# Kernel tuning notes

Measured on AMD Instinct MI355X. Metric: run time of the kernel, lower is better.

Reference implementation:

```python
import jax, jax.numpy as jnp
import numpy as np

N_ATOM = 100000
N_BOND = 400000
N_GLOBAL = 5000
IN = 128
OUT = 128
HEADS = 2
NEG_SLOPE = 0.2
BN_EPS = 1e-5


def setup_inputs() -> dict:
    key = jax.random.key(0)
    ks = jax.random.split(key, 12)
    atom_feats = jax.random.normal(ks[0], (N_ATOM, IN), jnp.float32)
    bond_feats = jax.random.normal(ks[1], (N_BOND, IN), jnp.float32)
    global_feats = jax.random.normal(ks[2], (N_GLOBAL, IN), jnp.float32)
    W_atom = jax.random.normal(ks[3], (IN, OUT * HEADS), jnp.float32) * 0.05
    W_bond = jax.random.normal(ks[4], (IN, OUT * HEADS), jnp.float32) * 0.05
    W_global = jax.random.normal(ks[5], (IN, OUT * HEADS), jnp.float32) * 0.05
    attn_l = jax.random.normal(ks[6], (1, HEADS, OUT), jnp.float32) * 0.1
    attn_r = jax.random.normal(ks[7], (1, HEADS, OUT), jnp.float32) * 0.1
    bn_gamma = jnp.ones((OUT,), jnp.float32)
    bn_beta = jnp.zeros((OUT,), jnp.float32)
    bond_src = jax.random.randint(ks[8], (N_BOND,), 0, N_ATOM, jnp.int32)
    # ensure every atom appears as a bond destination at least once (DGL-like semantics)
    bond_dst = jnp.concatenate([
        jnp.arange(N_ATOM, dtype=jnp.int32),
        jax.random.randint(ks[9], (N_BOND - N_ATOM,), 0, N_ATOM, jnp.int32),
    ])
    g2a_src = jax.random.randint(ks[10], (N_ATOM,), 0, N_GLOBAL, jnp.int32)
    return dict(atom_feats=atom_feats, bond_feats=bond_feats, global_feats=global_feats,
                W_atom=W_atom, W_bond=W_bond, W_global=W_global,
                attn_l=attn_l, attn_r=attn_r, bn_gamma=bn_gamma, bn_beta=bn_beta,
                bond_src=bond_src, bond_dst=bond_dst, g2a_src=g2a_src)


def _fwd(atom_feats, bond_feats, global_feats, W_atom, W_bond, W_global,
         attn_l, attn_r, bn_gamma, bn_beta, bond_src, bond_dst, g2a_src):
    lrelu = lambda x: jax.nn.leaky_relu(x, NEG_SLOPE)
    # projections -> [*, H, D]
    h = (atom_feats @ W_atom).reshape(-1, HEADS, OUT)      # [N,H,D]
    e = (bond_feats @ W_bond).reshape(-1, HEADS, OUT)      # [E,H,D]
    u = (global_feats @ W_global).reshape(-1, HEADS, OUT)  # [G,H,D]
    er = (h * attn_r).sum(-1)    # [N,H]
    el_h = (h * attn_l).sum(-1)  # [N,H]
    el_e = (e * attn_l).sum(-1)  # [E,H]
    el_u = (u * attn_l).sum(-1)  # [G,H]
    er_dst = er[bond_dst]                      # [E,H]
    eh = lrelu(el_h[bond_src] + er_dst)        # bond: u_add_v
    ee = lrelu(el_e + er_dst)                  # bond: e_add_v
    eu = lrelu(el_u[g2a_src] + er)             # g2a: u_add_v (dst = arange(N))
    # numerically-stable edge softmax over both edge types per destination atom
    emax_b = jax.ops.segment_max(jnp.maximum(eh, ee), bond_dst, num_segments=N_ATOM)
    emax = jnp.maximum(emax_b, eu)             # [N,H]
    eh = jnp.exp(eh - emax[bond_dst])
    ee = jnp.exp(ee - emax[bond_dst])
    eu = jnp.exp(eu - emax)
    esum = jax.ops.segment_sum(eh + ee, bond_dst, num_segments=N_ATOM) + eu  # [N,H]
    esum_dst = esum[bond_dst]
    alpha_h = eh / esum_dst    # [E,H]
    alpha_e = ee / esum_dst
    alpha_u = eu / esum        # [N,H]
    msg = h[bond_src] * alpha_h[:, :, None] + e * alpha_e[:, :, None]  # [E,H,D]
    out = jax.ops.segment_sum(msg, bond_dst, num_segments=N_ATOM)
    out = out + u[g2a_src] * alpha_u[:, :, None]   # [N,H,D]
    hN = out.mean(axis=1)                           # mean over heads -> [N,D]
    # BatchNorm1d (training-mode batch stats, biased var)
    mean = hN.mean(axis=0)
    var = ((hN - mean) ** 2).mean(axis=0)
    hN = (hN - mean) * jax.lax.rsqrt(var + BN_EPS) * bn_gamma + bn_beta
    return jax.nn.relu(hN)


def reference(atom_feats, bond_feats, global_feats, W_atom, W_bond, W_global,
              attn_l, attn_r, bn_gamma, bn_beta, bond_src, bond_dst, g2a_src):
    return _fwd(atom_feats, bond_feats, global_feats, W_atom, W_bond, W_global,
                attn_l, attn_r, bn_gamma, bn_beta, bond_src, bond_dst, g2a_src)
```

## Files before the change

### kernel.cpp

```cpp
#include <hip/hip_runtime.h>
#include <hip/hip_bf16.h>

#define NA 100000
#define NB 400000
#define NG 5000
#define NEG 0.2f
#define KDIM 512
#define CAP 32
#define FG_BLKS 782
#define KSC_BLKS 7891

typedef __attribute__((ext_vector_type(8))) short bf16x8;
typedef __attribute__((ext_vector_type(8))) unsigned short u16x8;
typedef __attribute__((ext_vector_type(4))) float f32x4;

__device__ __forceinline__ float lrelu(float x){ return x > 0.f ? x : NEG*x; }
__device__ __forceinline__ unsigned short f2bf(float f){
  unsigned u = __float_as_uint(f);
  u = (u + 0x7FFFu + ((u>>16)&1u)) >> 16;
  return (unsigned short)u;
}
__device__ __forceinline__ float bf2f(unsigned short s){
  return __uint_as_float(((unsigned)s) << 16);
}
__device__ __forceinline__ ushort2 pk2(float x, float y){
  __hip_bfloat162 t = __float22bfloat162_rn(make_float2(x, y));
  return *reinterpret_cast<ushort2*>(&t);
}

__global__ void kW(const float* __restrict__ Wa, const float* __restrict__ Wb,
                   const float* __restrict__ Wg, const float* __restrict__ glob,
                   const float* __restrict__ al, const float* __restrict__ ar,
                   unsigned short* wTa, unsigned short* wTb, unsigned short* wTu,
                   unsigned short* WcT, unsigned short* P){
  int blk = blockIdx.x;
  int tid = threadIdx.x;
  if (blk == 0){
    int k = tid >> 1, h = tid & 1;
    const float* wa = Wa + k*256 + h*128;
    const float* wb = Wb + k*256 + h*128;
    const float* wg = Wg + k*256 + h*128;
    const float* pl = al + h*128;
    const float* pr = ar + h*128;
    float sa=0.f, sra=0.f, se=0.f, su=0.f;
    for (int d=0; d<128; ++d){
      float L = pl[d], R = pr[d];
      sa  += wa[d]*L;  sra += wa[d]*R;
      se  += wb[d]*L;  su  += wg[d]*L;
    }
    wTa[h*128 + k]     = f2bf(sa);
    wTa[(2+h)*128 + k] = f2bf(sra);
    wTb[h*128 + k]     = f2bf(se);
    wTu[h*128 + k]     = f2bf(su);
    for (int idx = tid; idx < 14*128; idx += 256){
      int c = 2 + (idx >> 7), k2 = idx & 127;
      wTb[c*128 + k2] = 0;
      wTu[c*128 + k2] = 0;
      if (c >= 4) wTa[c*128 + k2] = 0;
    }
  } else if (blk <= 256){
    int idx = (blk-1)*256 + tid;
    int c = idx / KDIM, j = idx % KDIM;
    int part = j >> 7, k = j & 127;
    const float* W = (part < 2) ? Wa : Wb;
    int h = part & 1;
    WcT[(size_t)c*KDIM + j] = f2bf(0.5f * W[k*256 + h*128 + c]);
  } else {
    __shared__ float gl[8][128];
    int g0 = (blk-257)*8;
    #pragma unroll
    for (int r=0;r<4;++r){
      int idx = r*256+tid;
      gl[idx>>7][idx&127] = glob[(size_t)(g0 + (idx>>7))*128 + (idx&127)];
    }
    __syncthreads();
    float acc[8];
    #pragma unroll
    for (int g=0;g<8;++g) acc[g]=0.f;
    for (int k=0;k<128;++k){
      float wv = Wg[k*256 + tid];
      #pragma unroll
      for (int g=0;g<8;++g) acc[g] += gl[g][k]*wv;
    }
    #pragma unroll
    for (int g=0;g<8;++g)
      P[(size_t)(g0+g)*256 + tid] = f2bf(0.5f*acc[g]);
  }
}

__global__ __launch_bounds__(256) void kSC(
    const float* __restrict__ atom, const float* __restrict__ bond,
    const float* __restrict__ glob,
    const unsigned short* __restrict__ wTa, const unsigned short* __restrict__ wTb,
    const unsigned short* __restrict__ wTu,
    float* __restrict__ el_h, float* __restrict__ er,
    float* __restrict__ el_e, float* __restrict__ el_u,
    unsigned short* __restrict__ atomB, unsigned short* __restrict__ bondB){
  __shared__ unsigned short lds[4][16*128];
  const int wid = threadIdx.x >> 6;
  const int l = threadIdx.x & 63;
  const long rowbase = ((long)blockIdx.x*4 + wid) * 16;

  const float* feats; const unsigned short* wT; unsigned short* fb;
  long r0; long nrows; int type;
  if (rowbase < NA){            feats = atom; wT = wTa; fb = atomB; r0 = rowbase;          nrows = NA; type = 0; }
  else if (rowbase < NA+NB){    feats = bond; wT = wTb; fb = bondB; r0 = rowbase-NA;       nrows = NB; type = 1; }
  else {                        feats = glob; wT = wTu; fb = nullptr; r0 = rowbase-(NA+NB); nrows = NG; type = 2; }

  bf16x8 bfrag[4];
  #pragma unroll
  for (int kk=0;kk<4;++kk)
    bfrag[kk] = *reinterpret_cast<const bf16x8*>(wT + (size_t)(l&15)*128 + kk*32 + (l>>4)*8);

  unsigned short* wlds = lds[wid];
  const int j = l & 15;
  const int rl0 = l >> 4;
  #pragma unroll
  for (int i=0;i<4;++i){
    int rl = rl0 + i*4;
    long gr = r0 + rl;
    long grc = gr < nrows ? gr : (nrows-1);
    const float* src = feats + grc*128 + j*8;
    float4 x0 = *reinterpret_cast<const float4*>(src);
    float4 x1 = *reinterpret_cast<const float4*>(src+4);
    u16x8 w;
    ushort2 c0 = pk2(x0.x, x0.y), c1 = pk2(x0.z, x0.w);
    ushort2 c2 = pk2(x1.x, x1.y), c3 = pk2(x1.z, x1.w);
    w[0]=c0.x; w[1]=c0.y; w[2]=c1.x; w[3]=c1.y;
    w[4]=c2.x; w[5]=c2.y; w[6]=c3.x; w[7]=c3.y;
    *reinterpret_cast<u16x8*>(&wlds[rl*128 + ((j ^ (rl&7))*8)]) = w;
    if (fb && gr < nrows)
      *reinterpret_cast<u16x8*>(fb + grc*128 + j*8) = w;
  }
  __syncthreads();

  f32x4 acc = (f32x4){0.f,0.f,0.f,0.f};
  const int arow = l & 15;
  #pragma unroll
  for (int kk=0;kk<4;++kk){
    int ch = (kk*4 + (l>>4)) ^ (arow & 7);
    bf16x8 a = *reinterpret_cast<const bf16x8*>(&wlds[arow*128 + ch*8]);
    acc = __builtin_amdgcn_mfma_f32_16x16x32_bf16(a, bfrag[kk], acc, 0, 0, 0);
  }

  const int col = l & 15;
  if (col < 4 && (type == 0 || col < 2)){
    #pragma unroll
    for (int i=0;i<4;++i){
      long gr = r0 + (l>>4)*4 + i;
      if (gr < nrows){
        float v = acc[i];
        if (type == 0){
          if (col < 2) el_h[2*gr + col] = v;
          else         er[2*gr + col-2] = v;
        } else if (type == 1){
          el_e[2*gr + col] = v;
        } else {
          el_u[2*gr + col] = v;
        }
      }
    }
  }
}

__global__ void k4_edgeexp(const int* __restrict__ bsrc, const int* __restrict__ bdst,
                           const float* __restrict__ el_h, const float* __restrict__ er,
                           const float* __restrict__ el_e,
                           int2* __restrict__ slot_bs, float4* __restrict__ slot_e,
                           int* __restrict__ cursor, float* __restrict__ esum){
  int b = blockIdx.x*256 + threadIdx.x;
  if (b >= NB) return;
  int s = bsrc[b], d = bdst[b];
  float2 elh = *reinterpret_cast<const float2*>(&el_h[2*s]);
  float2 erd = *reinterpret_cast<const float2*>(&er[2*d]);
  float2 ele = *reinterpret_cast<const float2*>(&el_e[2*b]);
  float a0 = __expf(lrelu(elh.x + erd.x));
  float a1 = __expf(lrelu(elh.y + erd.y));
  float b0 = __expf(lrelu(ele.x + erd.x));
  float b1 = __expf(lrelu(ele.y + erd.y));
  int pos = atomicAdd(&cursor[d], 1);
  if (pos < CAP){
    slot_bs[(size_t)d*CAP + pos] = make_int2(b, s);
    slot_e [(size_t)d*CAP + pos] = make_float4(a0, a1, b0, b1);
  }
  atomicAdd(&esum[2*d],   a0 + b0);
  atomicAdd(&esum[2*d+1], a1 + b1);
}

__global__ void kPre(const int* __restrict__ cursor, const float* __restrict__ esum,
                     const float* __restrict__ el_u, const float* __restrict__ er,
                     const int* __restrict__ g2a,
                     float4* __restrict__ recF, int* __restrict__ recC){
  int n = blockIdx.x*256 + threadIdx.x;
  if (n >= NA) return;
  int cc = cursor[n]; cc = cc > CAP ? CAP : cc;
  int g = g2a[n];
  float2 elu = *reinterpret_cast<const float2*>(&el_u[2*g]);
  float2 ern = *reinterpret_cast<const float2*>(&er[2*n]);
  float u0 = __expf(lrelu(elu.x + ern.x));
  float u1 = __expf(lrelu(elu.y + ern.y));
  float iv0 = 1.f/(esum[2*n]   + u0);
  float iv1 = 1.f/(esum[2*n+1] + u1);
  recF[n] = make_float4(iv0, iv1, u0*iv0, u1*iv1);
  recC[n] = cc;
}

__global__ __launch_bounds__(512, 4) void kFG(
    const unsigned short* __restrict__ atomB,
    const unsigned short* __restrict__ bondB,
    const int2* __restrict__ slot_bs, const float4* __restrict__ slot_e,
    const float4* __restrict__ recF, const int* __restrict__ recC,
    const int* __restrict__ g2a,
    const unsigned short* __restrict__ WcT,
    const unsigned short* __restrict__ P,
    float* __restrict__ out, float* __restrict__ colsum, float* __restrict__ colsq){
  __shared__ unsigned short XA[128*256];
  __shared__ float au_s[128][2];
  const int tid = threadIdx.x;
  const int l  = tid & 63;
  const int li = tid & 15;
  const int gid = tid >> 4;
  const int w = tid >> 6;
  const int wr = w >> 2, wc = w & 3;
  const int gb = l & 48;
  const int n0 = blockIdx.x * 128;

  f32x4 acc[4][2];
  #pragma unroll
  for (int m=0;m<4;++m)
    #pragma unroll
    for (int nf=0;nf<2;++nf) acc[m][nf] = (f32x4){0.f,0.f,0.f,0.f};

  auto agg = [&](int phase){
    for (int t=0; t<4; ++t){
      int ln = gid + t*32;
      int n = n0 + ln;
      float a0[8], a1[8];
      #pragma unroll
      for (int k2=0;k2<8;++k2){ a0[k2]=0.f; a1[k2]=0.f; }
      int cc = 0; float iv0=0.f, iv1=0.f;
      if (n < NA){
        cc = recC[n];
        float4 rec = recF[n];
        iv0 = rec.x; iv1 = rec.y;
        if (phase==0 && li==0){ au_s[ln][0]=rec.z; au_s[ln][1]=rec.w; }
      }
      int idxA=0, idxB=0; float w0A=0.f,w1A=0.f,w0B=0.f,w1B=0.f;
      if (li < cc){
        int2 bs = slot_bs[(size_t)n*CAP + li];
        float4 e = slot_e[(size_t)n*CAP + li];
        idxA = phase ? bs.x : bs.y;
        w0A = phase ? e.z : e.x;
        w1A = phase ? e.w : e.y;
      }
      if (li+16 < cc){
        int2 bs = slot_bs[(size_t)n*CAP + li+16];
        float4 e = slot_e[(size_t)n*CAP + li+16];
        idxB = phase ? bs.x : bs.y;
        w0B = phase ? e.z : e.x;
        w1B = phase ? e.w : e.y;
      }
      const unsigned short* tbl = phase ? bondB : atomB;
      if (cc > 0){
        const int last = cc - 1;
        #define IDXJ(J) ({ int _jj = (J) <= last ? (J) : last; \
                           int _sl = gb + (_jj & 15); \
                           (_jj < 16) ? __shfl(idxA, _sl) : __shfl(idxB, _sl); })
        u16x8 x0 = *reinterpret_cast<const u16x8*>(tbl + (size_t)IDXJ(0)*128 + li*8);
        u16x8 x1 = *reinterpret_cast<const u16x8*>(tbl + (size_t)IDXJ(1)*128 + li*8);
        u16x8 x2 = *reinterpret_cast<const u16x8*>(tbl + (size_t)IDXJ(2)*128 + li*8);
        u16x8 x3 = *reinterpret_cast<const u16x8*>(tbl + (size_t)IDXJ(3)*128 + li*8);
        for (int j0 = 0; j0 < cc; j0 += 4){
          u16x8 y0=x0, y1=x1, y2=x2, y3=x3;
          x0 = *reinterpret_cast<const u16x8*>(tbl + (size_t)IDXJ(j0+4)*128 + li*8);
          x1 = *reinterpret_cast<const u16x8*>(tbl + (size_t)IDXJ(j0+5)*128 + li*8);
          x2 = *reinterpret_cast<const u16x8*>(tbl + (size_t)IDXJ(j0+6)*128 + li*8);
          x3 = *reinterpret_cast<const u16x8*>(tbl + (size_t)IDXJ(j0+7)*128 + li*8);
          #define CONSUME(YY, JJ) { \
            int _j = j0 + (JJ); \
            int _jc = _j <= last ? _j : last; \
            int _sl = gb + (_jc & 15); \
            float _w0 = (_jc < 16) ? __shfl(w0A, _sl) : __shfl(w0B, _sl); \
            float _w1 = (_jc < 16) ? __shfl(w1A, _sl) : __shfl(w1B, _sl); \
            float _c0 = (_j <= last) ? _w0*iv0 : 0.f; \
            float _c1 = (_j <= last) ? _w1*iv1 : 0.f; \
            _Pragma("unroll") \
            for (int k2=0;k2<8;++k2){ \
              float _v = bf2f((YY)[k2]); \
              a0[k2] += _c0*_v; a1[k2] += _c1*_v; \
            } }
          CONSUME(y0, 0)
          CONSUME(y1, 1)
          CONSUME(y2, 2)
          CONSUME(y3, 3)
          #undef CONSUME
        }
        #undef IDXJ
      }
      u16x8 o0, o1;
      #pragma unroll
      for (int k2=0;k2<8;++k2){ o0[k2]=f2bf(a0[k2]); o1[k2]=f2bf(a1[k2]); }
      *reinterpret_cast<u16x8*>(&XA[ln*256 + ((li   ) ^ (ln&7))*8]) = o0;
      *reinterpret_cast<u16x8*>(&XA[ln*256 + ((16+li) ^ (ln&7))*8]) = o1;
    }
  };

  auto gemm = [&](int phase){
    #pragma unroll
    for (int ks=0; ks<8; ++ks){
      bf16x8 av[4], bv[2];
      #pragma unroll
      for (int m=0;m<4;++m){
        int row = wr*64 + m*16 + (l&15);
        int ch = (ks*4 + (l>>4)) ^ (row&7);
        av[m] = *reinterpret_cast<const bf16x8*>(&XA[row*256 + ch*8]);
      }
      #pragma unroll
      for (int nf=0;nf<2;++nf){
        int col = wc*32 + nf*16 + (l&15);
        bv[nf] = *reinterpret_cast<const bf16x8*>(
            WcT + (size_t)col*KDIM + phase*256 + ks*32 + (l>>4)*8);
      }
      #pragma unroll
      for (int m=0;m<4;++m)
        #pragma unroll
        for (int nf=0;nf<2;++nf)
          acc[m][nf] = __builtin_amdgcn_mfma_f32_16x16x32_bf16(av[m], bv[nf], acc[m][nf], 0, 0, 0);
    }
  };

  agg(0);
  __syncthreads();
  gemm(0);
  __syncthreads();
  agg(1);
  __syncthreads();
  gemm(1);

  float s[2] = {0.f,0.f};
  float q[2] = {0.f,0.f};
  #pragma unroll
  for (int m=0;m<4;++m){
    #pragma unroll
    for (int i=0;i<4;++i){
      int row_l = wr*64 + m*16 + (l>>4)*4 + i;
      size_t row = (size_t)n0 + row_l;
      if (row < NA){
        float aux = au_s[row_l][0], auy = au_s[row_l][1];
        int g = g2a[row];
        const unsigned short* Pg = P + (size_t)g*256;
        #pragma unroll
        for (int nf=0;nf<2;++nf){
          int col = wc*32 + nf*16 + (l&15);
          float v = acc[m][nf][i] + aux*bf2f(Pg[col]) + auy*bf2f(Pg[128+col]);
          out[row*128 + col] = v;
          s[nf] += v; q[nf] += v*v;
        }
      }
    }
  }
  #pragma unroll
  for (int nf=0;nf<2;++nf){
    int col = wc*32 + nf*16 + (l&15);
    float sv = s[nf], qv = q[nf];
    sv += __shfl_xor(sv, 16); sv += __shfl_xor(sv, 32);
    qv += __shfl_xor(qv, 16); qv += __shfl_xor(qv, 32);
    if (l < 16){
      atomicAdd(&colsum[col], sv);
      atomicAdd(&colsq[col],  qv);
    }
  }
}

__global__ __launch_bounds__(256) void k11_bnrelu(float* __restrict__ out,
                            const float* __restrict__ colsum, const float* __restrict__ colsq,
                            const float* __restrict__ gamma, const float* __restrict__ beta){
  __shared__ float sc[128], sh[128];
  int t = threadIdx.x;
  if (t < 128){
    float mean = colsum[t] / (float)NA;
    float var = fmaxf(colsq[t] / (float)NA - mean*mean, 0.f);
    float s = gamma[t] * rsqrtf(var + 1e-5f);
    sc[t] = s;
    sh[t] = beta[t] - mean*s;
  }
  __syncthreads();
  int i = blockIdx.x*256 + t;
  float4 v = reinterpret_cast<float4*>(out)[i];
  int c0 = (i*4) & 127;
  v.x = fmaxf(0.f, v.x*sc[c0]   + sh[c0]);
  v.y = fmaxf(0.f, v.y*sc[c0+1] + sh[c0+1]);
  v.z = fmaxf(0.f, v.z*sc[c0+2] + sh[c0+2]);
  v.w = fmaxf(0.f, v.w*sc[c0+3] + sh[c0+3]);
  reinterpret_cast<float4*>(out)[i] = v;
}

extern "C" void kernel_launch(void* const* d_in, const int* in_sizes, int n_in,
                              void* d_out, int out_size, void* d_ws, size_t ws_size,
                              hipStream_t stream) {
  const float* atom = (const float*)d_in[0];
  const float* bond = (const float*)d_in[1];
  const float* glob = (const float*)d_in[2];
  const float* Wa   = (const float*)d_in[3];
  const float* Wb   = (const float*)d_in[4];
  const float* Wg   = (const float*)d_in[5];
  const float* al   = (const float*)d_in[6];
  const float* ar   = (const float*)d_in[7];
  const float* gamma= (const float*)d_in[8];
  const float* beta = (const float*)d_in[9];
  const int* bsrc   = (const int*)d_in[10];
  const int* bdst   = (const int*)d_in[11];
  const int* g2a    = (const int*)d_in[12];
  float* out = (float*)d_out;

  char* base = (char*)d_ws;
  size_t off = 0;
  auto carve = [&](size_t bytes)->void*{
    void* p = base + off;
    off = (off + bytes + 255) & ~(size_t)255;
    return p;
  };
  unsigned short* wTa = (unsigned short*)carve((size_t)16*128*2);
  unsigned short* wTb = (unsigned short*)carve((size_t)16*128*2);
  unsigned short* wTu = (unsigned short*)carve((size_t)16*128*2);
  unsigned short* WcT = (unsigned short*)carve((size_t)128*KDIM*2);
  unsigned short* P   = (unsigned short*)carve((size_t)NG*256*2);
  float* el_h = (float*)carve((size_t)NA*2*4);
  float* er   = (float*)carve((size_t)NA*2*4);
  float* el_e = (float*)carve((size_t)NB*2*4);
  float* el_u = (float*)carve((size_t)NG*2*4);
  float4* recF = (float4*)carve((size_t)NA*16);
  int*    recC = (int*)carve((size_t)NA*4);
  char* zr = (char*)carve((size_t)NA*2*4 + (size_t)NA*4 + 256*4);
  float* esum   = (float*)(zr);
  int*   cursor = (int*)(zr + (size_t)NA*2*4);
  float* colsum = (float*)(zr + (size_t)NA*2*4 + (size_t)NA*4);
  float* colsq  = colsum + 128;
  size_t zbytes = (size_t)NA*2*4 + (size_t)NA*4 + 256*4;
  int2*   slot_bs = (int2*)carve((size_t)NA*CAP*8);
  float4* slot_e  = (float4*)carve((size_t)NA*CAP*16);
  unsigned short* atomB = (unsigned short*)carve((size_t)NA*128*2);
  unsigned short* bondB = (unsigned short*)carve((size_t)NB*128*2);

  hipMemsetAsync(zr, 0, zbytes, stream);

  kW<<<882, 256, 0, stream>>>(Wa, Wb, Wg, glob, al, ar, wTa, wTb, wTu, WcT, P);

  kSC<<<KSC_BLKS, 256, 0, stream>>>(atom, bond, glob, wTa, wTb, wTu,
                                    el_h, er, el_e, el_u, atomB, bondB);

  k4_edgeexp<<<1563, 256, 0, stream>>>(bsrc, bdst, el_h, er, el_e,
                                       slot_bs, slot_e, cursor, esum);

  kPre<<<391, 256, 0, stream>>>(cursor, esum, el_u, er, g2a, recF, recC);

  kFG<<<FG_BLKS, 512, 0, stream>>>(atomB, bondB, slot_bs, slot_e, recF, recC,
                                   g2a, WcT, P, out, colsum, colsq);

  k11_bnrelu<<<12500, 256, 0, stream>>>(out, colsum, colsq, gamma, beta);
}
```

Before: 311.6 us.

## Sort atoms by in-degree bucket before fused aggregate-GEMM kernel

Adds a counting sort of atoms by their clamped in-degree (histogram in kPre, a single-thread scan, then a scatter) and has kFG process atoms in permuted order, writing results back to the original rows. Grouping nodes with similar degree is meant to even out per-wave aggregation work and reduce divergence inside 16-lane groups. In exchange it adds two small kernels, heavy atomics on 33 bins, and an extra indirection that makes output row writes and record reads non-contiguous.

Result: slower. 1.193 ms (+282.9%).

```diff
diff --git a/kernel.cpp b/kernel.cpp
--- a/kernel.cpp
+++ b/kernel.cpp
@@ -7,6 +7,7 @@
 #define NEG 0.2f
 #define KDIM 512
 #define CAP 32
+#define NBINS 33
 #define FG_BLKS 782
 #define KSC_BLKS 7891
 
@@ -190,7 +191,8 @@
 __global__ void kPre(const int* __restrict__ cursor, const float* __restrict__ esum,
                      const float* __restrict__ el_u, const float* __restrict__ er,
                      const int* __restrict__ g2a,
-                     float4* __restrict__ recF, int* __restrict__ recC){
+                     float4* __restrict__ recF, int* __restrict__ recC,
+                     int* __restrict__ binCnt){
   int n = blockIdx.x*256 + threadIdx.x;
   if (n >= NA) return;
   int cc = cursor[n]; cc = cc > CAP ? CAP : cc;
@@ -203,6 +205,23 @@
   float iv1 = 1.f/(esum[2*n+1] + u1);
   recF[n] = make_float4(iv0, iv1, u0*iv0, u1*iv1);
   recC[n] = cc;
+  atomicAdd(&binCnt[cc], 1);
+}
+
+__global__ void kScan(const int* __restrict__ binCnt, int* __restrict__ binOff){
+  if (threadIdx.x == 0){
+    int acc = 0;
+    for (int i=0;i<NBINS;++i){ binOff[i] = acc; acc += binCnt[i]; }
+  }
+}
+
+__global__ void kScat(const int* __restrict__ recC, const int* __restrict__ binOff,
+                      int* __restrict__ binCur, int* __restrict__ perm){
+  int n = blockIdx.x*256 + threadIdx.x;
+  if (n >= NA) return;
+  int cc = recC[n];
+  int pos = binOff[cc] + atomicAdd(&binCur[cc], 1);
+  perm[pos] = n;
 }
 
 __global__ __launch_bounds__(512, 4) void kFG(
@@ -210,12 +229,14 @@
     const unsigned short* __restrict__ bondB,
     const int2* __restrict__ slot_bs, const float4* __restrict__ slot_e,
     const float4* __restrict__ recF, const int* __restrict__ recC,
+    const int* __restrict__ perm,
     const int* __restrict__ g2a,
     const unsigned short* __restrict__ WcT,
     const unsigned short* __restrict__ P,
     float* __restrict__ out, float* __restrict__ colsum, float* __restrict__ colsq){
   __shared__ unsigned short XA[128*256];
   __shared__ float au_s[128][2];
+  __shared__ int   prm_s[128];
   const int tid = threadIdx.x;
   const int l  = tid & 63;
   const int li = tid & 15;
@@ -234,16 +255,18 @@
   auto agg = [&](int phase){
     for (int t=0; t<4; ++t){
       int ln = gid + t*32;
-      int n = n0 + ln;
+      int pn = n0 + ln;
       float a0[8], a1[8];
       #pragma unroll
       for (int k2=0;k2<8;++k2){ a0[k2]=0.f; a1[k2]=0.f; }
       int cc = 0; float iv0=0.f, iv1=0.f;
-      if (n < NA){
+      int n = 0;
+      if (pn < NA){
+        n = perm[pn];
         cc = recC[n];
         float4 rec = recF[n];
         iv0 = rec.x; iv1 = rec.y;
-        if (phase==0 && li==0){ au_s[ln][0]=rec.z; au_s[ln][1]=rec.w; }
+        if (phase==0 && li==0){ au_s[ln][0]=rec.z; au_s[ln][1]=rec.w; prm_s[ln]=n; }
       }
       int idxA=0, idxB=0; float w0A=0.f,w1A=0.f,w0B=0.f,w1B=0.f;
       if (li < cc){
@@ -344,8 +367,9 @@
     #pragma unroll
     for (int i=0;i<4;++i){
       int row_l = wr*64 + m*16 + (l>>4)*4 + i;
-      size_t row = (size_t)n0 + row_l;
-      if (row < NA){
+      int pn = n0 + row_l;
+      if (pn < NA){
+        size_t row = (size_t)prm_s[row_l];
         float aux = au_s[row_l][0], auy = au_s[row_l][1];
         int g = g2a[row];
         const unsigned short* Pg = P + (size_t)g*256;
@@ -431,12 +455,16 @@
   float* el_u = (float*)carve((size_t)NG*2*4);
   float4* recF = (float4*)carve((size_t)NA*16);
   int*    recC = (int*)carve((size_t)NA*4);
-  char* zr = (char*)carve((size_t)NA*2*4 + (size_t)NA*4 + 256*4);
+  int*    perm = (int*)carve((size_t)NA*4);
+  int*    binOff = (int*)carve(64*4);
+  size_t zbytes = (size_t)NA*2*4 + (size_t)NA*4 + 256*4 + 128*4;
+  char* zr = (char*)carve(zbytes);
   float* esum   = (float*)(zr);
   int*   cursor = (int*)(zr + (size_t)NA*2*4);
   float* colsum = (float*)(zr + (size_t)NA*2*4 + (size_t)NA*4);
   float* colsq  = colsum + 128;
-  size_t zbytes = (size_t)NA*2*4 + (size_t)NA*4 + 256*4;
+  int*   binCnt = (int*)(zr + (size_t)NA*2*4 + (size_t)NA*4 + 256*4);
+  int*   binCur = binCnt + 64;
   int2*   slot_bs = (int2*)carve((size_t)NA*CAP*8);
   float4* slot_e  = (float4*)carve((size_t)NA*CAP*16);
   unsigned short* atomB = (unsigned short*)carve((size_t)NA*128*2);
@@ -452,10 +480,12 @@
   k4_edgeexp<<<1563, 256, 0, stream>>>(bsrc, bdst, el_h, er, el_e,
                                        slot_bs, slot_e, cursor, esum);
 
-  kPre<<<391, 256, 0, stream>>>(cursor, esum, el_u, er, g2a, recF, recC);
+  kPre<<<391, 256, 0, stream>>>(cursor, esum, el_u, er, g2a, recF, recC, binCnt);
+  kScan<<<1, 64, 0, stream>>>(binCnt, binOff);
+  kScat<<<391, 256, 0, stream>>>(recC, binOff, binCur, perm);
 
   kFG<<<FG_BLKS, 512, 0, stream>>>(atomB, bondB, slot_bs, slot_e, recF, recC,
-                                   g2a, WcT, P, out, colsum, colsq);
+                                   perm, g2a, WcT, P, out, colsum, colsq);
 
   k11_bnrelu<<<12500, 256, 0, stream>>>(out, colsum, colsq, gamma, beta);
 }
```
